# Kernel optimization log

Hardware: AMD Instinct MI355X
Metric: run time of the kernel (lower is better)

Reference implementation:

```python
import jax, jax.numpy as jnp
import numpy as np

DIM = 512
HEADS = 8
DIM_HEAD = 64
INNER = HEADS * DIM_HEAD  # 512
B, N = 4, 2048
EPS = 1e-5
DIFF = 1.0


def setup_inputs() -> dict:
    key = jax.random.key(0)
    ks = jax.random.split(key, 8)
    s = 1.0 / np.sqrt(DIM)
    return {
        "x": jax.random.normal(ks[0], (B, N, DIM), dtype=jnp.float32),
        "ln_w": jnp.ones((DIM,), jnp.float32),
        "ln_b": jnp.zeros((DIM,), jnp.float32),
        "wq": jax.random.uniform(ks[1], (INNER, DIM), jnp.float32, -s, s),
        "wk": jax.random.uniform(ks[2], (INNER, DIM), jnp.float32, -s, s),
        "wv_v": jax.random.uniform(ks[3], (INNER, DIM), jnp.float32, -s, s),  # weight-norm direction
        "wv_g": jax.random.uniform(ks[4], (INNER,), jnp.float32, 0.5, 1.5),   # weight-norm magnitude g
        "w_out": jax.random.uniform(ks[5], (DIM, INNER), jnp.float32, -s, s),
    }


def reference(x, ln_w, ln_b, wq, wk, wv_v, wv_g, w_out):
    # LayerNorm over last dim
    mu = jnp.mean(x, axis=-1, keepdims=True)
    var = jnp.mean(jnp.square(x - mu), axis=-1, keepdims=True)
    xn = (x - mu) * jax.lax.rsqrt(var + EPS) * ln_w + ln_b

    # weight-norm for V projection: W = g * v / ||v||_row (norm over dim=1)
    wv = wv_g[:, None] * wv_v / jnp.linalg.norm(wv_v, axis=1, keepdims=True)

    def proj(w):  # [b n (h d)] -> [b h n d]
        t = jnp.einsum('bnc,ec->bne', xn, w)
        return t.reshape(x.shape[0], x.shape[1], HEADS, DIM_HEAD).transpose(0, 2, 1, 3)

    q, k, v = proj(wq), proj(wk), proj(wv)

    scale = DIM_HEAD ** -0.5
    dots = jnp.einsum('bhid,bhjd->bhij', q, k) * scale
    attn = jax.nn.softmax(dots, axis=-1)
    out = jnp.einsum('bhij,bhjd->bhid', DIFF * attn, v)  # diff-scaled AV
    out = out.transpose(0, 2, 1, 3).reshape(x.shape[0], x.shape[1], INNER)
    return jnp.einsum('bne,ce->bnc', out, w_out)
```

## Files before the change

### kernel.cpp

```cpp
#include <hip/hip_runtime.h>
#include <hip/hip_bf16.h>
#include <stdint.h>

typedef __attribute__((ext_vector_type(8))) __bf16 bf16x8;
typedef __attribute__((ext_vector_type(8))) short short8;
typedef __attribute__((ext_vector_type(4))) float f32x4;

#define C1_QSCALE 0.18033688011112042f

__device__ __forceinline__ unsigned short f2bf(float f) {
    union { float f; unsigned int u; } v; v.f = f;
    unsigned int r = v.u + 0x7fffu + ((v.u >> 16) & 1u);
    return (unsigned short)(r >> 16);
}

__device__ __forceinline__ unsigned int cvtpk(float lo, float hi) {
    unsigned int r;
    asm("v_cvt_pk_bf16_f32 %0, %1, %2" : "=v"(r) : "v"(lo), "v"(hi));
    return r;
}

__device__ __forceinline__ float fexp2(float x) {
    float r;
    asm("v_exp_f32 %0, %1" : "=v"(r) : "v"(x));
    return r;
}

__device__ __forceinline__ void gl_lds16(const void* g, void* l) {
    __builtin_amdgcn_global_load_lds(
        (const __attribute__((address_space(1))) unsigned int*)g,
        (__attribute__((address_space(3))) unsigned int*)l, 16, 0, 0);
}

__device__ __forceinline__ f32x4 mfma16(bf16x8 a, bf16x8 b, f32x4 c) {
    return __builtin_amdgcn_mfma_f32_16x16x32_bf16(a, b, c, 0, 0, 0);
}

__global__ __launch_bounds__(256) void ln_kernel(
    const float* __restrict__ x, const float* __restrict__ lw,
    const float* __restrict__ lb, unsigned short* __restrict__ xn)
{
    const int t = threadIdx.x, wv = t >> 6, l = t & 63;
    const int row = blockIdx.x * 4 + wv;
    const float* xr = x + (size_t)row * 512;
    const float4 a = *(const float4*)(xr + l*8);
    const float4 b = *(const float4*)(xr + l*8 + 4);
    float s  = (a.x + a.y) + (a.z + a.w) + (b.x + b.y) + (b.z + b.w);
    float sq = (a.x*a.x + a.y*a.y) + (a.z*a.z + a.w*a.w)
             + (b.x*b.x + b.y*b.y) + (b.z*b.z + b.w*b.w);
    #pragma unroll
    for (int m = 1; m < 64; m <<= 1) { s += __shfl_xor(s, m); sq += __shfl_xor(sq, m); }
    const float mean = s * (1.f/512.f);
    const float var  = sq * (1.f/512.f) - mean*mean;
    const float rs   = rsqrtf(var + 1e-5f);
    const float4 w0 = *(const float4*)(lw + l*8);
    const float4 w1 = *(const float4*)(lw + l*8 + 4);
    const float4 c0 = *(const float4*)(lb + l*8);
    const float4 c1 = *(const float4*)(lb + l*8 + 4);
    uint4 o;
    o.x = cvtpk((a.x-mean)*rs*w0.x + c0.x, (a.y-mean)*rs*w0.y + c0.y);
    o.y = cvtpk((a.z-mean)*rs*w0.z + c0.z, (a.w-mean)*rs*w0.w + c0.w);
    o.z = cvtpk((b.x-mean)*rs*w1.x + c1.x, (b.y-mean)*rs*w1.y + c1.y);
    o.w = cvtpk((b.z-mean)*rs*w1.z + c1.z, (b.w-mean)*rs*w1.w + c1.w);
    *(uint4*)(xn + (size_t)row*512 + l*8) = o;
}

__global__ void wprep(const float* __restrict__ wq, const float* __restrict__ wk,
                      const float* __restrict__ wv_v, const float* __restrict__ wv_g,
                      const float* __restrict__ w_out,
                      unsigned short* __restrict__ wqkv, unsigned short* __restrict__ woutb)
{
    __shared__ float red[4];
    const int row = blockIdx.x, t = threadIdx.x;
    if (row < 1536) {
        const float* src;
        float scale = 1.0f;
        if (row < 512) src = wq + (size_t)row*512;
        else if (row < 1024) src = wk + (size_t)(row-512)*512;
        else {
            src = wv_v + (size_t)(row-1024)*512;
            float2 v = *(const float2*)(src + t*2);
            float sq = v.x*v.x + v.y*v.y;
            #pragma unroll
            for (int m = 1; m < 64; m <<= 1) sq += __shfl_xor(sq, m);
            if ((t & 63) == 0) red[t >> 6] = sq;
            __syncthreads();
            scale = wv_g[row-1024] * rsqrtf(red[0]+red[1]+red[2]+red[3]);
        }
        float2 v = *(const float2*)(src + t*2);
        ushort2 o; o.x = f2bf(v.x*scale); o.y = f2bf(v.y*scale);
        *(ushort2*)(wqkv + (size_t)row*512 + t*2) = o;
    } else {
        const int r = row - 1536;
        float2 v = *(const float2*)(w_out + (size_t)r*512 + t*2);
        ushort2 o; o.x = f2bf(v.x); o.y = f2bf(v.y);
        *(ushort2*)(woutb + (size_t)r*512 + t*2) = o;
    }
}

template<int MODE, int BM, int BN>
__global__ __launch_bounds__(256) void gemm_nt(
    const unsigned short* __restrict__ A,
    const unsigned short* __restrict__ B,
    unsigned short* __restrict__ qo,
    unsigned short* __restrict__ ko,
    unsigned short* __restrict__ vo,
    float* __restrict__ outf)
{
    constexpr int MT = BM / 32;
    constexpr int NT = BN / 32;
    __shared__ __align__(16) unsigned char As[2][BM*128];
    __shared__ __align__(16) unsigned char Bs[2][BN*128];
    const int t = threadIdx.x;
    const int wv = t >> 6, l = t & 63;
    const int brow = blockIdx.x * BM;
    const int bcol = blockIdx.y * BN;
    const int wr = (wv >> 1) * (BM/2), wc = (wv & 1) * (BN/2);
    const int l15 = l & 15, l4 = l >> 4;
    const int rl = l >> 3, cbl = l & 7;

    const f32x4 fz = {0.f, 0.f, 0.f, 0.f};
    f32x4 acc[MT][NT];
    #pragma unroll
    for (int i = 0; i < MT; ++i)
        #pragma unroll
        for (int j = 0; j < NT; ++j) acc[i][j] = fz;

    auto STAGE = [&](int ks, int buf) {
        #pragma unroll
        for (int i = 0; i < MT; ++i) {
            const int c = wv*MT + i;
            const int row = c*8 + rl;
            const int scb = cbl ^ (row & 7);
            gl_lds16(A + (size_t)(brow+row)*512 + ks*64 + scb*8, &As[buf][c*1024]);
        }
        #pragma unroll
        for (int i = 0; i < NT; ++i) {
            const int c = wv*NT + i;
            const int row = c*8 + rl;
            const int scb = cbl ^ (row & 7);
            gl_lds16(B + (size_t)(bcol+row)*512 + ks*64 + scb*8, &Bs[buf][c*1024]);
        }
    };

    STAGE(0, 0);
    asm volatile("s_waitcnt vmcnt(0)" ::: "memory");
    __syncthreads();

    int cur = 0;
    for (int ks = 0; ks < 8; ++ks) {
        if (ks < 7) STAGE(ks + 1, cur ^ 1);
        #pragma unroll
        for (int kk = 0; kk < 2; ++kk) {
            bf16x8 af[MT], bfr[NT];
            #pragma unroll
            for (int mt = 0; mt < MT; ++mt) {
                const int row = wr + mt*16 + l15;
                const int cb = kk*4 + l4;
                af[mt] = *(const bf16x8*)(&As[cur][0] + row*128 + ((cb ^ (row & 7))*16));
            }
            #pragma unroll
            for (int nt = 0; nt < NT; ++nt) {
                const int row = wc + nt*16 + l15;
                const int cb = kk*4 + l4;
                bfr[nt] = *(const bf16x8*)(&Bs[cur][0] + row*128 + ((cb ^ (row & 7))*16));
            }
            __builtin_amdgcn_s_setprio(1);
            #pragma unroll
            for (int mt = 0; mt < MT; ++mt)
                #pragma unroll
                for (int nt = 0; nt < NT; ++nt)
                    acc[mt][nt] = mfma16(af[mt], bfr[nt], acc[mt][nt]);
            __builtin_amdgcn_s_setprio(0);
        }
        asm volatile("s_waitcnt vmcnt(0)" ::: "memory");
        __syncthreads();
        cur ^= 1;
    }

    if (MODE == 1) {
        #pragma unroll
        for (int mt = 0; mt < MT; ++mt)
            #pragma unroll
            for (int nt = 0; nt < NT; ++nt)
                #pragma unroll
                for (int r = 0; r < 4; ++r) {
                    const int grow = brow + wr + mt*16 + l4*4 + r;
                    const int gcol = bcol + wc + nt*16 + l15;
                    outf[(size_t)grow*512 + gcol] = acc[mt][nt][r];
                }
    } else if (bcol < 1024) {
        const bool isq = (bcol < 512);
        unsigned short* dst = isq ? qo : ko;
        const int csub = isq ? bcol : bcol - 512;
        const float scl = isq ? C1_QSCALE : 1.0f;
        #pragma unroll
        for (int mt = 0; mt < MT; ++mt)
            #pragma unroll
            for (int nt = 0; nt < NT; ++nt)
                #pragma unroll
                for (int r = 0; r < 4; ++r) {
                    const int grow = brow + wr + mt*16 + l4*4 + r;
                    const int gcol = csub + wc + nt*16 + l15;
                    const int h = gcol >> 6, d = gcol & 63;
                    const int bb = grow >> 11, n = grow & 2047;
                    dst[(((size_t)bb*8 + h)*2048 + n)*64 + d] = f2bf(acc[mt][nt][r]*scl);
                }
    } else {
        #pragma unroll
        for (int mt = 0; mt < MT; ++mt) {
            const int grow0 = brow + wr + mt*16 + l4*4;
            const int bb = grow0 >> 11;
            const int nb = (grow0 & 2047) & ~63;
            const int sigma0 = (mt>>1)*32 + l4*8 + (mt&1)*4;
            #pragma unroll
            for (int nt = 0; nt < NT; ++nt) {
                const int gcol = (bcol - 1024) + wc + nt*16 + l15;
                const int h = gcol >> 6, d = gcol & 63;
                uint2 ov;
                ov.x = cvtpk(acc[mt][nt][0], acc[mt][nt][1]);
                ov.y = cvtpk(acc[mt][nt][2], acc[mt][nt][3]);
                *(uint2*)(vo + ((size_t)(bb*8 + h)*64 + d)*2048 + nb + sigma0) = ov;
            }
        }
    }
}

__global__ __launch_bounds__(256, 4) void flash_attn(
    const unsigned short* __restrict__ Q,
    const unsigned short* __restrict__ K,
    const unsigned short* __restrict__ Vt,
    unsigned short* __restrict__ AO)
{
    __shared__ __align__(16) unsigned char Ks[3][8192];
    __shared__ __align__(16) unsigned char Vs[2][8192];
    const int t = threadIdx.x, wv = t >> 6, l = t & 63;
    const int l15 = l & 15, l4 = l >> 4;
    const int rl = l >> 3, cbl = l & 7;
    const int bh = blockIdx.x;
    const int q0 = blockIdx.y * 64;
    const size_t base = (size_t)bh * 2048 * 64;
    const int b = bh >> 3, h = bh & 7;

    bf16x8 qf[2];
    #pragma unroll
    for (int kk = 0; kk < 2; ++kk)
        qf[kk] = *(const bf16x8*)(Q + base + (size_t)(q0 + wv*16 + l15)*64 + kk*32 + 8*l4);

    const f32x4 fz = {0.f,0.f,0.f,0.f};
    f32x4 acco[4];
    float lr = 0.f;
    #pragma unroll
    for (int dn = 0; dn < 4; ++dn) acco[dn] = fz;

    auto STAGE_K = [&](int kv, int buf) {
        #pragma unroll
        for (int i = 0; i < 2; ++i) {
            const int c = wv*2 + i;
            const int row = c*8 + rl;
            const int scb = cbl ^ (row & 7);
            gl_lds16(K + base + (size_t)(kv + row)*64 + scb*8, &Ks[buf][c*1024]);
        }
    };
    auto STAGE_V = [&](int kv, int buf) {
        #pragma unroll
        for (int i = 0; i < 2; ++i) {
            const int c = wv*2 + i;
            const int row = c*8 + rl;
            const int scb = cbl ^ (row & 7);
            gl_lds16(Vt + base + (size_t)row*2048 + kv + scb*8, &Vs[buf][c*1024]);
        }
    };

    STAGE_V(0, 0);
    STAGE_K(0, 0);
    STAGE_K(64, 1);

    int kb = 0, vb = 0;
    for (int it = 0; it < 32; ++it) {
        asm volatile("s_waitcnt vmcnt(4)" ::: "memory");
        __builtin_amdgcn_s_barrier();

        STAGE_V(((it + 1) & 31) * 64, vb ^ 1);
        STAGE_K(((it + 2) & 31) * 64, kb >= 1 ? kb - 1 : 2);

        bf16x8 kf[4][2];
        #pragma unroll
        for (int nt = 0; nt < 4; ++nt)
            #pragma unroll
            for (int kk = 0; kk < 2; ++kk) {
                const int row = nt*16 + l15;
                const int cb = kk*4 + l4;
                kf[nt][kk] = *(const bf16x8*)(&Ks[kb][0] + row*128 + ((cb ^ (row & 7))*16));
            }
        f32x4 st[4];
        __builtin_amdgcn_s_setprio(1);
        #pragma unroll
        for (int nt = 0; nt < 4; ++nt) {
            st[nt] = mfma16(kf[nt][0], qf[0], fz);
            st[nt] = mfma16(kf[nt][1], qf[1], st[nt]);
        }
        __builtin_amdgcn_s_setprio(0);

        float p[4][4];
        float rsum = 0.f;
        #pragma unroll
        for (int nt = 0; nt < 4; ++nt) {
            #pragma unroll
            for (int r = 0; r < 4; ++r) p[nt][r] = fexp2(st[nt][r]);
            rsum += (p[nt][0] + p[nt][1]) + (p[nt][2] + p[nt][3]);
        }
        bf16x8 pb[2];
        #pragma unroll
        for (int kh = 0; kh < 2; ++kh) {
            union { unsigned int u[4]; bf16x8 v; } pu;
            pu.u[0] = cvtpk(p[2*kh][0],   p[2*kh][1]);
            pu.u[1] = cvtpk(p[2*kh][2],   p[2*kh][3]);
            pu.u[2] = cvtpk(p[2*kh+1][0], p[2*kh+1][1]);
            pu.u[3] = cvtpk(p[2*kh+1][2], p[2*kh+1][3]);
            pb[kh] = pu.v;
        }
        rsum += __shfl_xor(rsum, 16);
        rsum += __shfl_xor(rsum, 32);
        lr += rsum;

        asm volatile("s_waitcnt vmcnt(6)" ::: "memory");
        __builtin_amdgcn_s_barrier();

        __builtin_amdgcn_s_setprio(1);
        #pragma unroll
        for (int dn = 0; dn < 4; ++dn)
            #pragma unroll
            for (int kh = 0; kh < 2; ++kh) {
                const int row = dn*16 + l15;
                const int cb = kh*4 + l4;
                const bf16x8 vf = *(const bf16x8*)(&Vs[vb][0] + row*128 + ((cb ^ (row & 7))*16));
                acco[dn] = mfma16(vf, pb[kh], acco[dn]);
            }
        __builtin_amdgcn_s_setprio(0);

        kb = (kb == 2) ? 0 : kb + 1;
        vb ^= 1;
    }

    const float inv = 1.f / lr;
    const size_t nrow = (size_t)b*2048 + q0 + wv*16 + l15;
    #pragma unroll
    for (int dn = 0; dn < 4; ++dn) {
        uint2 ov;
        ov.x = cvtpk(acco[dn][0]*inv, acco[dn][1]*inv);
        ov.y = cvtpk(acco[dn][2]*inv, acco[dn][3]*inv);
        *(uint2*)(AO + nrow*512 + h*64 + dn*16 + l4*4) = ov;
    }
}

extern "C" void kernel_launch(void* const* d_in, const int* in_sizes, int n_in,
                              void* d_out, int out_size, void* d_ws, size_t ws_size,
                              hipStream_t stream)
{
    const float* x     = (const float*)d_in[0];
    const float* ln_w  = (const float*)d_in[1];
    const float* ln_b  = (const float*)d_in[2];
    const float* wq    = (const float*)d_in[3];
    const float* wk    = (const float*)d_in[4];
    const float* wv_v  = (const float*)d_in[5];
    const float* wv_g  = (const float*)d_in[6];
    const float* w_out = (const float*)d_in[7];
    float* out = (float*)d_out;
    char* ws = (char*)d_ws;

    unsigned short* xn    = (unsigned short*)(ws);
    unsigned short* ao    = (unsigned short*)(ws);
    unsigned short* wqkv  = (unsigned short*)(ws +  8388608);
    unsigned short* woutb = (unsigned short*)(ws +  9961472);
    unsigned short* q     = (unsigned short*)(ws + 10485760);
    unsigned short* k     = (unsigned short*)(ws + 18874368);
    unsigned short* vt    = (unsigned short*)(ws + 27262976);

    ln_kernel<<<dim3(2048), dim3(256), 0, stream>>>(x, ln_w, ln_b, xn);
    wprep<<<dim3(2048), dim3(256), 0, stream>>>(wq, wk, wv_v, wv_g, w_out, wqkv, woutb);
    gemm_nt<0,128,128><<<dim3(64, 12), dim3(256), 0, stream>>>(xn, wqkv, q, k, vt, (float*)nullptr);
    flash_attn<<<dim3(32, 32), dim3(256), 0, stream>>>(q, k, vt, ao);
    gemm_nt<1,64,64><<<dim3(128, 8), dim3(256), 0, stream>>>(ao, woutb,
        (unsigned short*)nullptr, (unsigned short*)nullptr, (unsigned short*)nullptr, out);
}
```

Baseline: 164.5 us.

## Merge prep kernels, drop mid-loop attention barrier, defer row-sum shuffles, widen out-proj tile

LayerNorm and weight preparation are merged into one launch to save a kernel launch and its tail. In the flash-attention loop, the second wait-and-barrier before the PV MFMAs is removed. The top-of-loop wait is tightened to vmcnt(2) so both K and V for the current iteration are resident at that single barrier. Row-sum cross-lane shuffles move out of the loop and run once at the end. The output projection switches to 128x64 tiles with half the blocks, trading parallelism for more reuse per block.

Result: faster. 160.1 us (-2.7%).

```diff
diff --git a/kernel.cpp b/kernel.cpp
--- a/kernel.cpp
+++ b/kernel.cpp
@@ -36,65 +36,66 @@
     return __builtin_amdgcn_mfma_f32_16x16x32_bf16(a, b, c, 0, 0, 0);
 }
 
-__global__ __launch_bounds__(256) void ln_kernel(
+__global__ __launch_bounds__(256) void pre_kernel(
     const float* __restrict__ x, const float* __restrict__ lw,
-    const float* __restrict__ lb, unsigned short* __restrict__ xn)
+    const float* __restrict__ lb, unsigned short* __restrict__ xn,
+    const float* __restrict__ wq, const float* __restrict__ wk,
+    const float* __restrict__ wv_v, const float* __restrict__ wv_g,
+    const float* __restrict__ w_out,
+    unsigned short* __restrict__ wqkv, unsigned short* __restrict__ woutb)
 {
-    const int t = threadIdx.x, wv = t >> 6, l = t & 63;
-    const int row = blockIdx.x * 4 + wv;
-    const float* xr = x + (size_t)row * 512;
-    const float4 a = *(const float4*)(xr + l*8);
-    const float4 b = *(const float4*)(xr + l*8 + 4);
-    float s  = (a.x + a.y) + (a.z + a.w) + (b.x + b.y) + (b.z + b.w);
-    float sq = (a.x*a.x + a.y*a.y) + (a.z*a.z + a.w*a.w)
-             + (b.x*b.x + b.y*b.y) + (b.z*b.z + b.w*b.w);
-    #pragma unroll
-    for (int m = 1; m < 64; m <<= 1) { s += __shfl_xor(s, m); sq += __shfl_xor(sq, m); }
-    const float mean = s * (1.f/512.f);
-    const float var  = sq * (1.f/512.f) - mean*mean;
-    const float rs   = rsqrtf(var + 1e-5f);
-    const float4 w0 = *(const float4*)(lw + l*8);
-    const float4 w1 = *(const float4*)(lw + l*8 + 4);
-    const float4 c0 = *(const float4*)(lb + l*8);
-    const float4 c1 = *(const float4*)(lb + l*8 + 4);
-    uint4 o;
-    o.x = cvtpk((a.x-mean)*rs*w0.x + c0.x, (a.y-mean)*rs*w0.y + c0.y);
-    o.y = cvtpk((a.z-mean)*rs*w0.z + c0.z, (a.w-mean)*rs*w0.w + c0.w);
-    o.z = cvtpk((b.x-mean)*rs*w1.x + c1.x, (b.y-mean)*rs*w1.y + c1.y);
-    o.w = cvtpk((b.z-mean)*rs*w1.z + c1.z, (b.w-mean)*rs*w1.w + c1.w);
-    *(uint4*)(xn + (size_t)row*512 + l*8) = o;
-}
-
-__global__ void wprep(const float* __restrict__ wq, const float* __restrict__ wk,
-                      const float* __restrict__ wv_v, const float* __restrict__ wv_g,
-                      const float* __restrict__ w_out,
-                      unsigned short* __restrict__ wqkv, unsigned short* __restrict__ woutb)
-{
-    __shared__ float red[4];
-    const int row = blockIdx.x, t = threadIdx.x;
-    if (row < 1536) {
-        const float* src;
-        float scale = 1.0f;
-        if (row < 512) src = wq + (size_t)row*512;
-        else if (row < 1024) src = wk + (size_t)(row-512)*512;
-        else {
-            src = wv_v + (size_t)(row-1024)*512;
+    const int t = threadIdx.x;
+    if (blockIdx.x < 2048) {
+        const int wv = t >> 6, l = t & 63;
+        const int row = blockIdx.x * 4 + wv;
+        const float* xr = x + (size_t)row * 512;
+        const float4 a = *(const float4*)(xr + l*8);
+        const float4 b = *(const float4*)(xr + l*8 + 4);
+        float s  = (a.x + a.y) + (a.z + a.w) + (b.x + b.y) + (b.z + b.w);
+        float sq = (a.x*a.x + a.y*a.y) + (a.z*a.z + a.w*a.w)
+                 + (b.x*b.x + b.y*b.y) + (b.z*b.z + b.w*b.w);
+        #pragma unroll
+        for (int m = 1; m < 64; m <<= 1) { s += __shfl_xor(s, m); sq += __shfl_xor(sq, m); }
+        const float mean = s * (1.f/512.f);
+        const float var  = sq * (1.f/512.f) - mean*mean;
+        const float rs   = rsqrtf(var + 1e-5f);
+        const float4 w0 = *(const float4*)(lw + l*8);
+        const float4 w1 = *(const float4*)(lw + l*8 + 4);
+        const float4 c0 = *(const float4*)(lb + l*8);
+        const float4 c1 = *(const float4*)(lb + l*8 + 4);
+        uint4 o;
+        o.x = cvtpk((a.x-mean)*rs*w0.x + c0.x, (a.y-mean)*rs*w0.y + c0.y);
+        o.y = cvtpk((a.z-mean)*rs*w0.z + c0.z, (a.w-mean)*rs*w0.w + c0.w);
+        o.z = cvtpk((b.x-mean)*rs*w1.x + c1.x, (b.y-mean)*rs*w1.y + c1.y);
+        o.w = cvtpk((b.z-mean)*rs*w1.z + c1.z, (b.w-mean)*rs*w1.w + c1.w);
+        *(uint4*)(xn + (size_t)row*512 + l*8) = o;
+    } else {
+        __shared__ float red[4];
+        const int row = blockIdx.x - 2048;
+        if (row < 1536) {
+            const float* src;
+            float scale = 1.0f;
+            if (row < 512) src = wq + (size_t)row*512;
+            else if (row < 1024) src = wk + (size_t)(row-512)*512;
+            else {
+                src = wv_v + (size_t)(row-1024)*512;
+                float2 v = *(const float2*)(src + t*2);
+                float sq = v.x*v.x + v.y*v.y;
+                #pragma unroll
+                for (int m = 1; m < 64; m <<= 1) sq += __shfl_xor(sq, m);
+                if ((t & 63) == 0) red[t >> 6] = sq;
+                __syncthreads();
+                scale = wv_g[row-1024] * rsqrtf(red[0]+red[1]+red[2]+red[3]);
+            }
             float2 v = *(const float2*)(src + t*2);
-            float sq = v.x*v.x + v.y*v.y;
-            #pragma unroll
-            for (int m = 1; m < 64; m <<= 1) sq += __shfl_xor(sq, m);
-            if ((t & 63) == 0) red[t >> 6] = sq;
-            __syncthreads();
-            scale = wv_g[row-1024] * rsqrtf(red[0]+red[1]+red[2]+red[3]);
-        }
-        float2 v = *(const float2*)(src + t*2);
-        ushort2 o; o.x = f2bf(v.x*scale); o.y = f2bf(v.y*scale);
-        *(ushort2*)(wqkv + (size_t)row*512 + t*2) = o;
-    } else {
-        const int r = row - 1536;
-        float2 v = *(const float2*)(w_out + (size_t)r*512 + t*2);
-        ushort2 o; o.x = f2bf(v.x); o.y = f2bf(v.y);
-        *(ushort2*)(woutb + (size_t)r*512 + t*2) = o;
+            ushort2 o; o.x = f2bf(v.x*scale); o.y = f2bf(v.y*scale);
+            *(ushort2*)(wqkv + (size_t)row*512 + t*2) = o;
+        } else {
+            const int r = row - 1536;
+            float2 v = *(const float2*)(w_out + (size_t)r*512 + t*2);
+            ushort2 o; o.x = f2bf(v.x); o.y = f2bf(v.y);
+            *(ushort2*)(woutb + (size_t)r*512 + t*2) = o;
+        }
     }
 }
 
@@ -249,7 +250,7 @@
 
     const f32x4 fz = {0.f,0.f,0.f,0.f};
     f32x4 acco[4];
-    float lr = 0.f;
+    float lrp = 0.f;
     #pragma unroll
     for (int dn = 0; dn < 4; ++dn) acco[dn] = fz;
 
@@ -278,7 +279,7 @@
 
     int kb = 0, vb = 0;
     for (int it = 0; it < 32; ++it) {
-        asm volatile("s_waitcnt vmcnt(4)" ::: "memory");
+        asm volatile("s_waitcnt vmcnt(2)" ::: "memory");
         __builtin_amdgcn_s_barrier();
 
         STAGE_V(((it + 1) & 31) * 64, vb ^ 1);
@@ -303,13 +304,16 @@
         __builtin_amdgcn_s_setprio(0);
 
         float p[4][4];
-        float rsum = 0.f;
-        #pragma unroll
-        for (int nt = 0; nt < 4; ++nt) {
+        #pragma unroll
+        for (int nt = 0; nt < 4; ++nt)
             #pragma unroll
             for (int r = 0; r < 4; ++r) p[nt][r] = fexp2(st[nt][r]);
-            rsum += (p[nt][0] + p[nt][1]) + (p[nt][2] + p[nt][3]);
-        }
+        float s0 = (p[0][0]+p[0][1]) + (p[0][2]+p[0][3]);
+        float s1 = (p[1][0]+p[1][1]) + (p[1][2]+p[1][3]);
+        float s2 = (p[2][0]+p[2][1]) + (p[2][2]+p[2][3]);
+        float s3 = (p[3][0]+p[3][1]) + (p[3][2]+p[3][3]);
+        lrp += (s0 + s1) + (s2 + s3);
+
         bf16x8 pb[2];
         #pragma unroll
         for (int kh = 0; kh < 2; ++kh) {
@@ -320,12 +324,6 @@
             pu.u[3] = cvtpk(p[2*kh+1][2], p[2*kh+1][3]);
             pb[kh] = pu.v;
         }
-        rsum += __shfl_xor(rsum, 16);
-        rsum += __shfl_xor(rsum, 32);
-        lr += rsum;
-
-        asm volatile("s_waitcnt vmcnt(6)" ::: "memory");
-        __builtin_amdgcn_s_barrier();
 
         __builtin_amdgcn_s_setprio(1);
         #pragma unroll
@@ -343,6 +341,9 @@
         vb ^= 1;
     }
 
+    float lr = lrp;
+    lr += __shfl_xor(lr, 16);
+    lr += __shfl_xor(lr, 32);
     const float inv = 1.f / lr;
     const size_t nrow = (size_t)b*2048 + q0 + wv*16 + l15;
     #pragma unroll
@@ -377,10 +378,10 @@
     unsigned short* k     = (unsigned short*)(ws + 18874368);
     unsigned short* vt    = (unsigned short*)(ws + 27262976);
 
-    ln_kernel<<<dim3(2048), dim3(256), 0, stream>>>(x, ln_w, ln_b, xn);
-    wprep<<<dim3(2048), dim3(256), 0, stream>>>(wq, wk, wv_v, wv_g, w_out, wqkv, woutb);
+    pre_kernel<<<dim3(4096), dim3(256), 0, stream>>>(x, ln_w, ln_b, xn,
+        wq, wk, wv_v, wv_g, w_out, wqkv, woutb);
     gemm_nt<0,128,128><<<dim3(64, 12), dim3(256), 0, stream>>>(xn, wqkv, q, k, vt, (float*)nullptr);
     flash_attn<<<dim3(32, 32), dim3(256), 0, stream>>>(q, k, vt, ao);
-    gemm_nt<1,64,64><<<dim3(128, 8), dim3(256), 0, stream>>>(ao, woutb,
+    gemm_nt<1,128,64><<<dim3(64, 8), dim3(256), 0, stream>>>(ao, woutb,
         (unsigned short*)nullptr, (unsigned short*)nullptr, (unsigned short*)nullptr, out);
 }
```
